# Performance work log

Measured on AMD Instinct MI355X. Metric: run time of the kernel, lower is better.

## Reference

```python
import jax, jax.numpy as jnp
import numpy as np

N = 100000   # nodes
E = 1600000  # edges
IN = 128     # input feature dim
HID = 64     # hidden = IN // 2
OUT = 8      # output_size
B = 16384    # lookup batch


def sage_conv(x, src, dst, W_l, W_r, b, n):
    # PyG SAGEConv (aggr='mean', root_weight=True):
    # out = lin_l(mean_{j in N(i)} x_j) + lin_r(x_i)
    msgs = x[src]                                              # [E, F] gather
    agg = jax.ops.segment_sum(msgs, dst, num_segments=n)       # [N, F] scatter-add
    deg = jax.ops.segment_sum(jnp.ones((src.shape[0],), x.dtype), dst, num_segments=n)
    mean = agg / jnp.maximum(deg, 1.0)[:, None]                # zero-degree -> 0
    return mean @ W_l + x @ W_r + b


def setup_inputs() -> dict:
    key = jax.random.key(0)
    ks = jax.random.split(key, 10)
    node_feats = jax.random.normal(ks[0], (N, IN), dtype=jnp.float32)
    edge_index = jax.random.randint(ks[1], (2, E), 0, N, dtype=jnp.int64)
    idx = jax.random.randint(ks[2], (B,), 0, N, dtype=jnp.int64)
    dropout_mask = jax.random.uniform(ks[3], (N, HID), dtype=jnp.float32)
    s1 = 1.0 / np.sqrt(IN)
    s2 = 1.0 / np.sqrt(HID)
    W1_l = jax.random.normal(ks[4], (IN, HID), dtype=jnp.float32) * s1
    W1_r = jax.random.normal(ks[5], (IN, HID), dtype=jnp.float32) * s1
    b1 = jnp.zeros((HID,), dtype=jnp.float32)
    W2_l = jax.random.normal(ks[6], (HID, OUT), dtype=jnp.float32) * s2
    W2_r = jax.random.normal(ks[7], (HID, OUT), dtype=jnp.float32) * s2
    b2 = jnp.zeros((OUT,), dtype=jnp.float32)
    return {"node_feats": node_feats, "edge_index": edge_index, "idx": idx,
            "dropout_mask": dropout_mask, "W1_l": W1_l, "W1_r": W1_r, "b1": b1,
            "W2_l": W2_l, "W2_r": W2_r, "b2": b2}


def reference(node_feats, edge_index, idx, dropout_mask, W1_l, W1_r, b1, W2_l, W2_r, b2):
    n = node_feats.shape[0]
    src, dst = edge_index[0], edge_index[1]
    h = sage_conv(node_feats, src, dst, W1_l, W1_r, b1, n)     # [N, HID]
    h = jax.nn.relu(h)
    keep = (dropout_mask > 0.5).astype(h.dtype)                # F.dropout p=0.5
    h = h * keep * 2.0                                         # inverted dropout scale 1/(1-p)
    emb = sage_conv(h, src, dst, W2_l, W2_r, b2, n)            # [N, OUT]
    return emb[idx]                                            # [B, OUT]
```

## Files before the change

kernel.cpp:

```cpp
#include <hip/hip_runtime.h>
#include <hip/hip_fp16.h>

#define IN_F 128
#define HID_F 64
#define OUT_F 8

#define BSHIFT 7
#define BGRAN 128
#define BCAP 2688
#define NBUK_MAX 784
#define CHUNK 4096
#define EPT (CHUNK / 256)
#define CEPT ((BCAP + 255) / 256)

typedef _Float16 f16x8 __attribute__((ext_vector_type(8)));
typedef float f32x4 __attribute__((ext_vector_type(4)));

__global__ __launch_bounds__(256) void prep(
    const float* __restrict__ Wl, const float* __restrict__ Wr,
    _Float16* __restrict__ Wt, int* __restrict__ bcur, int nbuk) {
  int blk = blockIdx.x;
  if (blk < 16) {
    int i = blk * 256 + threadIdx.x;
    int n = i & 127;
    int k4 = (i >> 7) * 4;
    _Float16 hv[4];
#pragma unroll
    for (int j = 0; j < 4; ++j) {
      float v = (n < HID_F) ? Wl[(k4 + j) * HID_F + n]
                            : Wr[(k4 + j) * HID_F + (n - HID_F)];
      hv[j] = (_Float16)v;
    }
    *(uint2*)(Wt + (size_t)n * IN_F + k4) = *(uint2*)hv;
  } else {
    for (int i = threadIdx.x; i < nbuk; i += 256) bcur[i] = i * BCAP;
  }
}

__global__ __launch_bounds__(256) void bucket_scatter(
    const int* __restrict__ src, const int* __restrict__ dst,
    int* __restrict__ bcur, int* __restrict__ ebuf, int n_edges) {
  __shared__ int hist[NBUK_MAX];
  __shared__ int base[NBUK_MAX];
  int t = threadIdx.x;
  for (int i = t; i < NBUK_MAX; i += 256) hist[i] = 0;
  __syncthreads();
  int e0 = blockIdx.x * CHUNK;
  int pk[EPT];
  int bk[EPT];
  int rk[EPT];
#pragma unroll
  for (int k = 0; k < EPT; ++k) {
    int e = e0 + k * 256 + t;
    if (e < n_edges) {
      int s = src[e];
      int d = dst[e];
      bk[k] = d >> BSHIFT;
      pk[k] = ((d & (BGRAN - 1)) << 24) | s;
      rk[k] = atomicAdd(&hist[bk[k]], 1);
    } else {
      bk[k] = -1;
    }
  }
  __syncthreads();
  for (int i = t; i < NBUK_MAX; i += 256) {
    int c = hist[i];
    base[i] = c ? atomicAdd(&bcur[i], c) : 0;
  }
  __syncthreads();
#pragma unroll
  for (int k = 0; k < EPT; ++k) {
    if (bk[k] >= 0) ebuf[base[bk[k]] + rk[k]] = pk[k];
  }
}

__global__ __launch_bounds__(256) void bucket_csr(
    const int* __restrict__ ebuf, const int* __restrict__ bcur,
    uint2* __restrict__ nd, int* __restrict__ csr_src, int n_nodes) {
  __shared__ int hist[BGRAN];
  __shared__ int excl_s[BGRAN];
  __shared__ int lds_src[BCAP];
  int b = blockIdx.x;
  int t = threadIdx.x;
  if (t < BGRAN) hist[t] = 0;
  __syncthreads();
  int beg = b * BCAP;
  int cnt = bcur[b] - beg;
  int pk[CEPT];
  int rk[CEPT];
#pragma unroll
  for (int u = 0; u < CEPT; ++u) {
    int j = t + u * 256;
    if (j < cnt) {
      pk[u] = ebuf[beg + j];
      rk[u] = atomicAdd(&hist[(unsigned)pk[u] >> 24], 1);
    } else {
      pk[u] = -1;
    }
  }
  __syncthreads();
  if (t < 64) {
    int h0 = hist[2 * t];
    int h1 = hist[2 * t + 1];
    int ps = h0 + h1;
#pragma unroll
    for (int dd = 1; dd < 64; dd <<= 1) {
      int u = __shfl_up(ps, dd);
      if (t >= dd) ps += u;
    }
    excl_s[2 * t] = ps - h1 - h0;
    excl_s[2 * t + 1] = ps - h1;
  }
  __syncthreads();
  if (t < BGRAN) {
    int node = b * BGRAN + t;
    if (node < n_nodes)
      nd[node] = make_uint2((unsigned)(beg + excl_s[t]), (unsigned)hist[t]);
  }
#pragma unroll
  for (int u = 0; u < CEPT; ++u) {
    if (pk[u] != -1) {
      int bin = (unsigned)pk[u] >> 24;
      lds_src[excl_s[bin] + rk[u]] = pk[u] & 0xFFFFFF;
    }
  }
  __syncthreads();
  for (int j = t; j < cnt; j += 256) csr_src[beg + j] = lds_src[j];
}

#define K1_ROWS 64
#define XSH 136
__global__ __launch_bounds__(256) void k1_proj(
    const float* __restrict__ x,
    const _Float16* __restrict__ Wt,
    const float* __restrict__ b1,
    __half* __restrict__ y1h,
    __half* __restrict__ r1h,
    int n_nodes) {
  __shared__ _Float16 XS[K1_ROWS * XSH];
  int tid = threadIdx.x;
  int w = tid >> 6;
  int lane = tid & 63;
  int n0 = blockIdx.x * K1_ROWS;
  int m = lane & 15;
  int quad = lane >> 4;

  f16x8 af[2][4];
#pragma unroll
  for (int ti = 0; ti < 2; ++ti) {
    int t = w + ti * 4;
#pragma unroll
    for (int kk = 0; kk < 4; ++kk)
      af[ti][kk] = *(const f16x8*)(Wt + (size_t)(t * 16 + m) * IN_F + kk * 32 + quad * 8);
  }
  float4 b1v = *(const float4*)(b1 + w * 16 + quad * 4);

#pragma unroll
  for (int p = 0; p < 8; ++p) {
    int i = tid + p * 256;
    int row = i >> 5;
    int k4 = (i & 31) * 4;
    int gs = min(n0 + row, n_nodes - 1);
    float4 v = *(const float4*)(x + (size_t)gs * IN_F + k4);
    _Float16 hv[4] = {(_Float16)v.x, (_Float16)v.y, (_Float16)v.z, (_Float16)v.w};
    *(uint2*)&XS[row * XSH + k4] = *(uint2*)hv;
  }
  __syncthreads();

#pragma unroll
  for (int rt = 0; rt < 4; ++rt) {
    f32x4 acc0 = f32x4{0.f, 0.f, 0.f, 0.f};
    f32x4 acc1 = f32x4{0.f, 0.f, 0.f, 0.f};
#pragma unroll
    for (int kk = 0; kk < 4; ++kk) {
      f16x8 bx = *(const f16x8*)&XS[(rt * 16 + m) * XSH + kk * 32 + quad * 8];
      acc0 = __builtin_amdgcn_mfma_f32_16x16x32_f16(af[0][kk], bx, acc0, 0, 0, 0);
      acc1 = __builtin_amdgcn_mfma_f32_16x16x32_f16(af[1][kk], bx, acc1, 0, 0, 0);
    }
    int node = n0 + rt * 16 + m;
    if (node < n_nodes) {
      __half hy[4], hr[4];
#pragma unroll
      for (int r = 0; r < 4; ++r) {
        hy[r] = __float2half(acc0[r]);
        hr[r] = __float2half(acc1[r] + ((const float*)&b1v)[r]);
      }
      *(uint2*)(y1h + (size_t)node * HID_F + w * 16 + quad * 4) = *(uint2*)hy;
      *(uint2*)(r1h + (size_t)node * HID_F + w * 16 + quad * 4) = *(uint2*)hr;
    }
  }
}

__global__ __launch_bounds__(256) void agg1_fused(
    const __half* __restrict__ y1h,
    const __half* __restrict__ r1h,
    const uint2* __restrict__ nd,
    const int* __restrict__ csr_src,
    const float* __restrict__ mask,
    __half* __restrict__ h_h,
    int n_nodes) {
  int node = (blockIdx.x * blockDim.x + threadIdx.x) >> 6;
  int lane = threadIdx.x & 63;
  if (node >= n_nodes) return;
  int nu = __builtin_amdgcn_readfirstlane(node);
  int q = lane >> 4;
  int f4 = lane & 15;

  uint2 be = nd[nu];
  size_t o = (size_t)nu * HID_F + f4 * 4;
  uint2 rg = *(const uint2*)(r1h + o);
  float4 mrow = *(const float4*)(mask + (size_t)nu * HID_F + f4 * 4);

  int beg = (int)be.x;
  int d = (int)be.y;
  const int* cp = csr_src + beg;
  const char* yb = (const char*)y1h;
  unsigned foff = (unsigned)(f4 * 8);

  float a0 = 0.f, a1 = 0.f, a2 = 0.f, a3 = 0.f;

#define FLUSH(hx, hy)                       \
  {                                         \
    float2 fx = __half22float2(hx);         \
    float2 fy = __half22float2(hy);         \
    a0 += fx.x; a1 += fx.y;                 \
    a2 += fy.x; a3 += fy.y;                 \
  }

  int j = 0;
  for (; j + 32 <= d; j += 32) {
    unsigned s0 = (unsigned)cp[j + q];
    unsigned s1 = (unsigned)cp[j + 4 + q];
    unsigned s2 = (unsigned)cp[j + 8 + q];
    unsigned s3 = (unsigned)cp[j + 12 + q];
    unsigned s4 = (unsigned)cp[j + 16 + q];
    unsigned s5 = (unsigned)cp[j + 20 + q];
    unsigned s6 = (unsigned)cp[j + 24 + q];
    unsigned s7 = (unsigned)cp[j + 28 + q];
    uint2 g0 = *(const uint2*)(yb + ((s0 << 7) + foff));
    uint2 g1 = *(const uint2*)(yb + ((s1 << 7) + foff));
    uint2 g2 = *(const uint2*)(yb + ((s2 << 7) + foff));
    uint2 g3 = *(const uint2*)(yb + ((s3 << 7) + foff));
    uint2 g4 = *(const uint2*)(yb + ((s4 << 7) + foff));
    uint2 g5 = *(const uint2*)(yb + ((s5 << 7) + foff));
    uint2 g6 = *(const uint2*)(yb + ((s6 << 7) + foff));
    uint2 g7 = *(const uint2*)(yb + ((s7 << 7) + foff));
    __half2 hx = *(const __half2*)&g0.x;
    __half2 hy = *(const __half2*)&g0.y;
    hx = __hadd2(hx, *(const __half2*)&g1.x);
    hy = __hadd2(hy, *(const __half2*)&g1.y);
    hx = __hadd2(hx, *(const __half2*)&g2.x);
    hy = __hadd2(hy, *(const __half2*)&g2.y);
    hx = __hadd2(hx, *(const __half2*)&g3.x);
    hy = __hadd2(hy, *(const __half2*)&g3.y);
    hx = __hadd2(hx, *(const __half2*)&g4.x);
    hy = __hadd2(hy, *(const __half2*)&g4.y);
    hx = __hadd2(hx, *(const __half2*)&g5.x);
    hy = __hadd2(hy, *(const __half2*)&g5.y);
    hx = __hadd2(hx, *(const __half2*)&g6.x);
    hy = __hadd2(hy, *(const __half2*)&g6.y);
    hx = __hadd2(hx, *(const __half2*)&g7.x);
    hy = __hadd2(hy, *(const __half2*)&g7.y);
    FLUSH(hx, hy)
  }
  if (j + 16 <= d) {
    unsigned s0 = (unsigned)cp[j + q];
    unsigned s1 = (unsigned)cp[j + 4 + q];
    unsigned s2 = (unsigned)cp[j + 8 + q];
    unsigned s3 = (unsigned)cp[j + 12 + q];
    uint2 g0 = *(const uint2*)(yb + ((s0 << 7) + foff));
    uint2 g1 = *(const uint2*)(yb + ((s1 << 7) + foff));
    uint2 g2 = *(const uint2*)(yb + ((s2 << 7) + foff));
    uint2 g3 = *(const uint2*)(yb + ((s3 << 7) + foff));
    __half2 hx = *(const __half2*)&g0.x;
    __half2 hy = *(const __half2*)&g0.y;
    hx = __hadd2(hx, *(const __half2*)&g1.x);
    hy = __hadd2(hy, *(const __half2*)&g1.y);
    hx = __hadd2(hx, *(const __half2*)&g2.x);
    hy = __hadd2(hy, *(const __half2*)&g2.y);
    hx = __hadd2(hx, *(const __half2*)&g3.x);
    hy = __hadd2(hy, *(const __half2*)&g3.y);
    FLUSH(hx, hy)
    j += 16;
  }
  if (j < d) {
    int dm = d - 1;
    int e0 = j + q, e1 = j + 4 + q, e2 = j + 8 + q, e3 = j + 12 + q;
    unsigned s0 = (unsigned)cp[min(e0, dm)];
    unsigned s1 = (unsigned)cp[min(e1, dm)];
    unsigned s2 = (unsigned)cp[min(e2, dm)];
    unsigned s3 = (unsigned)cp[min(e3, dm)];
    uint2 g0 = *(const uint2*)(yb + ((s0 << 7) + foff));
    uint2 g1 = *(const uint2*)(yb + ((s1 << 7) + foff));
    uint2 g2 = *(const uint2*)(yb + ((s2 << 7) + foff));
    uint2 g3 = *(const uint2*)(yb + ((s3 << 7) + foff));
    uint2 zz = make_uint2(0u, 0u);
    if (e0 >= d) g0 = zz;
    if (e1 >= d) g1 = zz;
    if (e2 >= d) g2 = zz;
    if (e3 >= d) g3 = zz;
    __half2 hx = *(const __half2*)&g0.x;
    __half2 hy = *(const __half2*)&g0.y;
    hx = __hadd2(hx, *(const __half2*)&g1.x);
    hy = __hadd2(hy, *(const __half2*)&g1.y);
    hx = __hadd2(hx, *(const __half2*)&g2.x);
    hy = __hadd2(hy, *(const __half2*)&g2.y);
    hx = __hadd2(hx, *(const __half2*)&g3.x);
    hy = __hadd2(hy, *(const __half2*)&g3.y);
    FLUSH(hx, hy)
  }
#undef FLUSH

  a0 += __shfl_xor(a0, 16); a0 += __shfl_xor(a0, 32);
  a1 += __shfl_xor(a1, 16); a1 += __shfl_xor(a1, 32);
  a2 += __shfl_xor(a2, 16); a2 += __shfl_xor(a2, 32);
  a3 += __shfl_xor(a3, 16); a3 += __shfl_xor(a3, 32);
  if (q == 0) {
    float inv = 1.0f / fmaxf((float)d, 1.0f);
    float2 r01 = __half22float2(*(const __half2*)&rg.x);
    float2 r23 = __half22float2(*(const __half2*)&rg.y);
    float vx = fmaxf(a0 * inv + r01.x, 0.f);
    float vy = fmaxf(a1 * inv + r01.y, 0.f);
    float vz = fmaxf(a2 * inv + r23.x, 0.f);
    float vw = fmaxf(a3 * inv + r23.y, 0.f);
    vx = (mrow.x > 0.5f) ? vx * 2.f : 0.f;
    vy = (mrow.y > 0.5f) ? vy * 2.f : 0.f;
    vz = (mrow.z > 0.5f) ? vz * 2.f : 0.f;
    vw = (mrow.w > 0.5f) ? vw * 2.f : 0.f;
    __half hh[4] = {__float2half(vx), __float2half(vy),
                    __float2half(vz), __float2half(vw)};
    *(uint2*)(h_h + o) = *(uint2*)hh;
  }
}

__global__ __launch_bounds__(256) void k3b_z(
    const __half* __restrict__ h_h,
    const float* __restrict__ W2l,
    __half* __restrict__ z,
    int n_nodes) {
  __shared__ float WS[HID_F][OUT_F];
  int tid = threadIdx.x;
  if (tid < 128) {
    float4 w = *(const float4*)(W2l + tid * 4);
    *(float4*)&WS[tid >> 1][(tid & 1) * 4] = w;
  }
  __syncthreads();
  int node = blockIdx.x * blockDim.x + tid;
  if (node >= n_nodes) return;
  const __half* hr = h_h + (size_t)node * HID_F;
  float acc[8] = {0, 0, 0, 0, 0, 0, 0, 0};
  for (int k = 0; k < HID_F; k += 8) {
    uint4 hv = *(const uint4*)(hr + k);
    float2 f0 = __half22float2(*(const __half2*)&hv.x);
    float2 f1 = __half22float2(*(const __half2*)&hv.y);
    float2 f2 = __half22float2(*(const __half2*)&hv.z);
    float2 f3 = __half22float2(*(const __half2*)&hv.w);
    float hh[8] = {f0.x, f0.y, f1.x, f1.y, f2.x, f2.y, f3.x, f3.y};
#pragma unroll
    for (int j = 0; j < 8; ++j) {
      float4 w0 = *(const float4*)&WS[k + j][0];
      float4 w1 = *(const float4*)&WS[k + j][4];
      acc[0] += hh[j] * w0.x; acc[1] += hh[j] * w0.y;
      acc[2] += hh[j] * w0.z; acc[3] += hh[j] * w0.w;
      acc[4] += hh[j] * w1.x; acc[5] += hh[j] * w1.y;
      acc[6] += hh[j] * w1.z; acc[7] += hh[j] * w1.w;
    }
  }
  __half hz[8];
#pragma unroll
  for (int j = 0; j < 8; ++j) hz[j] = __float2half(acc[j]);
  *(uint4*)(z + (size_t)node * OUT_F) = *(uint4*)hz;
}

__global__ __launch_bounds__(256) void out_fused(
    const int* __restrict__ idx,
    const __half* __restrict__ z,
    const uint2* __restrict__ nd,
    const int* __restrict__ csr_src,
    const __half* __restrict__ h_h,
    const float* __restrict__ W2r,
    const float* __restrict__ b2,
    float* __restrict__ out,
    int n_batch) {
  int b = (blockIdx.x * blockDim.x + threadIdx.x) >> 6;
  int lane = threadIdx.x & 63;
  if (b >= n_batch) return;
  int bu = __builtin_amdgcn_readfirstlane(b);
  int i = idx[bu];
  int iu = __builtin_amdgcn_readfirstlane(i);
  int e8 = lane >> 3;
  int o = lane & 7;
  uint2 be = nd[iu];
  uint4 hv = *(const uint4*)(h_h + (size_t)iu * HID_F + e8 * 8);
  int beg = (int)be.x;
  int d = (int)be.y;
  const int* cp = csr_src + beg;
  const char* zb = (const char*)z;
  unsigned ooff = (unsigned)(o * 2);
  float acc = 0.f;
  int j = e8;
  for (; j + 8 < d; j += 16) {
    unsigned s0 = (unsigned)cp[j];
    unsigned s1 = (unsigned)cp[j + 8];
    float z0 = __half2float(*(const __half*)(zb + ((s0 << 4) + ooff)));
    float z1 = __half2float(*(const __half*)(zb + ((s1 << 4) + ooff)));
    acc += z0 + z1;
  }
  if (j < d) {
    unsigned s0 = (unsigned)cp[j];
    acc += __half2float(*(const __half*)(zb + ((s0 << 4) + ooff)));
  }
  float dv = fmaxf((float)d, 1.0f);
  float v = acc / dv;
  float2 f0 = __half22float2(*(const __half2*)&hv.x);
  float2 f1 = __half22float2(*(const __half2*)&hv.y);
  float2 f2 = __half22float2(*(const __half2*)&hv.z);
  float2 f3 = __half22float2(*(const __half2*)&hv.w);
  float hh[8] = {f0.x, f0.y, f1.x, f1.y, f2.x, f2.y, f3.x, f3.y};
#pragma unroll
  for (int jj = 0; jj < 8; ++jj) {
    int k = e8 * 8 + jj;
    v += hh[jj] * W2r[k * OUT_F + o];
  }
  v += __shfl_xor(v, 8);
  v += __shfl_xor(v, 16);
  v += __shfl_xor(v, 32);
  if (e8 == 0) out[(size_t)b * OUT_F + o] = v + b2[o];
}

extern "C" void kernel_launch(void* const* d_in, const int* in_sizes, int n_in,
                              void* d_out, int out_size, void* d_ws, size_t ws_size,
                              hipStream_t stream) {
  const float* x    = (const float*)d_in[0];
  const int*   ei   = (const int*)d_in[1];
  const int*   idx  = (const int*)d_in[2];
  const float* mask = (const float*)d_in[3];
  const float* W1l  = (const float*)d_in[4];
  const float* W1r  = (const float*)d_in[5];
  const float* b1   = (const float*)d_in[6];
  const float* W2l  = (const float*)d_in[7];
  const float* W2r  = (const float*)d_in[8];
  const float* b2   = (const float*)d_in[9];
  float* out = (float*)d_out;

  int n_nodes = in_sizes[0] / IN_F;
  int n_edges = in_sizes[1] / 2;
  int n_batch = in_sizes[2];
  const int* src = ei;
  const int* dst = ei + n_edges;

  int nbuk = (n_nodes + BGRAN - 1) / BGRAN;
  int nchunk = (n_edges + CHUNK - 1) / CHUNK;

  char* ws = (char*)d_ws;
  size_t off = 0;
  __half* y1h = (__half*)(ws + off); off += (size_t)n_nodes * HID_F * 2;
  __half* r1h = (__half*)(ws + off); off += (size_t)n_nodes * HID_F * 2;
  __half* h_h = (__half*)(ws + off); off += (size_t)n_nodes * HID_F * 2;
  __half* z   = (__half*)(ws + off); off += (size_t)n_nodes * OUT_F * 2;
  _Float16* Wt = (_Float16*)(ws + off); off += (size_t)IN_F * IN_F * 2;
  int* ebuf    = (int*)(ws + off); off += (size_t)nbuk * BCAP * 4;
  int* csr_src = (int*)(ws + off); off += (size_t)nbuk * BCAP * 4;
  uint2* nd    = (uint2*)(ws + off); off += (size_t)n_nodes * 8;
  int* bcur    = (int*)(ws + off); off += NBUK_MAX * 4;

  prep<<<17, 256, 0, stream>>>(W1l, W1r, Wt, bcur, nbuk);
  bucket_scatter<<<nchunk, 256, 0, stream>>>(src, dst, bcur, ebuf, n_edges);
  k1_proj<<<(n_nodes + K1_ROWS - 1) / K1_ROWS, 256, 0, stream>>>(
      x, Wt, b1, y1h, r1h, n_nodes);
  bucket_csr<<<nbuk, 256, 0, stream>>>(ebuf, bcur, nd, csr_src, n_nodes);

  {
    long long th = (long long)n_nodes * HID_F;
    agg1_fused<<<(int)((th + 255) / 256), 256, 0, stream>>>(
        y1h, r1h, nd, csr_src, mask, h_h, n_nodes);
  }

  k3b_z<<<(n_nodes + 255) / 256, 256, 0, stream>>>(h_h, W2l, z, n_nodes);
  {
    long long th = (long long)n_batch * 64;
    out_fused<<<(int)((th + 255) / 256), 256, 0, stream>>>(
        idx, z, nd, csr_src, h_h, W2r, b2, out, n_batch);
  }
}
```

Measured before the change: 224.0 us.

## Persistent multi-node waves in agg1 with prefetched neighbor indices and packed dropout bits

agg1_fused now runs a fixed pool of waves, each handling several consecutive nodes. It prefetches the next node's CSR range and first 16 neighbor indices while the current node aggregates, to hide index-load latency. The dropout mask is packed into 64-bit bitmasks inside bucket_scatter, so agg1 reads 8 bytes per node instead of 256. The 32-wide unrolled gather loop is reduced to 16-wide, which lowers memory-level parallelism per wave. Fewer waves also means less latency hiding through occupancy.

New measurement: 236.3 us. 1.05x slower.

```diff
diff --git a/kernel.cpp b/kernel.cpp
--- a/kernel.cpp
+++ b/kernel.cpp
@@ -39,7 +39,9 @@
 
 __global__ __launch_bounds__(256) void bucket_scatter(
     const int* __restrict__ src, const int* __restrict__ dst,
-    int* __restrict__ bcur, int* __restrict__ ebuf, int n_edges) {
+    int* __restrict__ bcur, int* __restrict__ ebuf,
+    const float* __restrict__ mask, unsigned long long* __restrict__ mbits,
+    int n_edges, int n_nodes) {
   __shared__ int hist[NBUK_MAX];
   __shared__ int base[NBUK_MAX];
   int t = threadIdx.x;
@@ -71,6 +73,28 @@
 #pragma unroll
   for (int k = 0; k < EPT; ++k) {
     if (bk[k] >= 0) ebuf[base[bk[k]] + rk[k]] = pk[k];
+  }
+
+  int mpb = (n_nodes + (int)gridDim.x - 1) / (int)gridDim.x;
+  int nb0 = blockIdx.x * mpb;
+  int lim = min(nb0 + mpb, n_nodes);
+  int w = t >> 6;
+  int ln = t & 63;
+  for (int nn = nb0 + w * 4; nn < lim; nn += 16) {
+    float m0 = (nn + 0 < lim) ? mask[(size_t)(nn + 0) * HID_F + ln] : 0.f;
+    float m1 = (nn + 1 < lim) ? mask[(size_t)(nn + 1) * HID_F + ln] : 0.f;
+    float m2 = (nn + 2 < lim) ? mask[(size_t)(nn + 2) * HID_F + ln] : 0.f;
+    float m3 = (nn + 3 < lim) ? mask[(size_t)(nn + 3) * HID_F + ln] : 0.f;
+    unsigned long long b0 = __ballot(m0 > 0.5f);
+    unsigned long long b1 = __ballot(m1 > 0.5f);
+    unsigned long long b2 = __ballot(m2 > 0.5f);
+    unsigned long long b3 = __ballot(m3 > 0.5f);
+    if (ln == 0) {
+      if (nn + 0 < lim) mbits[nn + 0] = b0;
+      if (nn + 1 < lim) mbits[nn + 1] = b1;
+      if (nn + 2 < lim) mbits[nn + 2] = b2;
+      if (nn + 3 < lim) mbits[nn + 3] = b3;
+    }
   }
 }
 
@@ -196,141 +220,141 @@
     const __half* __restrict__ r1h,
     const uint2* __restrict__ nd,
     const int* __restrict__ csr_src,
-    const float* __restrict__ mask,
+    const unsigned long long* __restrict__ mbits,
     __half* __restrict__ h_h,
-    int n_nodes) {
-  int node = (blockIdx.x * blockDim.x + threadIdx.x) >> 6;
+    int n_nodes, int npw) {
+  int wid = (blockIdx.x * 256 + threadIdx.x) >> 6;
   int lane = threadIdx.x & 63;
-  if (node >= n_nodes) return;
-  int nu = __builtin_amdgcn_readfirstlane(node);
   int q = lane >> 4;
   int f4 = lane & 15;
-
-  uint2 be = nd[nu];
-  size_t o = (size_t)nu * HID_F + f4 * 4;
-  uint2 rg = *(const uint2*)(r1h + o);
-  float4 mrow = *(const float4*)(mask + (size_t)nu * HID_F + f4 * 4);
-
-  int beg = (int)be.x;
-  int d = (int)be.y;
-  const int* cp = csr_src + beg;
+  int n0 = wid * npw;
+  if (n0 >= n_nodes) return;
+  int nend = min(n0 + npw, n_nodes);
   const char* yb = (const char*)y1h;
   unsigned foff = (unsigned)(f4 * 8);
 
-  float a0 = 0.f, a1 = 0.f, a2 = 0.f, a3 = 0.f;
-
-#define FLUSH(hx, hy)                       \
-  {                                         \
-    float2 fx = __half22float2(hx);         \
-    float2 fy = __half22float2(hy);         \
-    a0 += fx.x; a1 += fx.y;                 \
-    a2 += fy.x; a3 += fy.y;                 \
-  }
-
-  int j = 0;
-  for (; j + 32 <= d; j += 32) {
-    unsigned s0 = (unsigned)cp[j + q];
-    unsigned s1 = (unsigned)cp[j + 4 + q];
-    unsigned s2 = (unsigned)cp[j + 8 + q];
-    unsigned s3 = (unsigned)cp[j + 12 + q];
-    unsigned s4 = (unsigned)cp[j + 16 + q];
-    unsigned s5 = (unsigned)cp[j + 20 + q];
-    unsigned s6 = (unsigned)cp[j + 24 + q];
-    unsigned s7 = (unsigned)cp[j + 28 + q];
-    uint2 g0 = *(const uint2*)(yb + ((s0 << 7) + foff));
-    uint2 g1 = *(const uint2*)(yb + ((s1 << 7) + foff));
-    uint2 g2 = *(const uint2*)(yb + ((s2 << 7) + foff));
-    uint2 g3 = *(const uint2*)(yb + ((s3 << 7) + foff));
-    uint2 g4 = *(const uint2*)(yb + ((s4 << 7) + foff));
-    uint2 g5 = *(const uint2*)(yb + ((s5 << 7) + foff));
-    uint2 g6 = *(const uint2*)(yb + ((s6 << 7) + foff));
-    uint2 g7 = *(const uint2*)(yb + ((s7 << 7) + foff));
-    __half2 hx = *(const __half2*)&g0.x;
-    __half2 hy = *(const __half2*)&g0.y;
-    hx = __hadd2(hx, *(const __half2*)&g1.x);
-    hy = __hadd2(hy, *(const __half2*)&g1.y);
-    hx = __hadd2(hx, *(const __half2*)&g2.x);
-    hy = __hadd2(hy, *(const __half2*)&g2.y);
-    hx = __hadd2(hx, *(const __half2*)&g3.x);
-    hy = __hadd2(hy, *(const __half2*)&g3.y);
-    hx = __hadd2(hx, *(const __half2*)&g4.x);
-    hy = __hadd2(hy, *(const __half2*)&g4.y);
-    hx = __hadd2(hx, *(const __half2*)&g5.x);
-    hy = __hadd2(hy, *(const __half2*)&g5.y);
-    hx = __hadd2(hx, *(const __half2*)&g6.x);
-    hy = __hadd2(hy, *(const __half2*)&g6.y);
-    hx = __hadd2(hx, *(const __half2*)&g7.x);
-    hy = __hadd2(hy, *(const __half2*)&g7.y);
-    FLUSH(hx, hy)
-  }
-  if (j + 16 <= d) {
-    unsigned s0 = (unsigned)cp[j + q];
-    unsigned s1 = (unsigned)cp[j + 4 + q];
-    unsigned s2 = (unsigned)cp[j + 8 + q];
-    unsigned s3 = (unsigned)cp[j + 12 + q];
-    uint2 g0 = *(const uint2*)(yb + ((s0 << 7) + foff));
-    uint2 g1 = *(const uint2*)(yb + ((s1 << 7) + foff));
-    uint2 g2 = *(const uint2*)(yb + ((s2 << 7) + foff));
-    uint2 g3 = *(const uint2*)(yb + ((s3 << 7) + foff));
-    __half2 hx = *(const __half2*)&g0.x;
-    __half2 hy = *(const __half2*)&g0.y;
-    hx = __hadd2(hx, *(const __half2*)&g1.x);
-    hy = __hadd2(hy, *(const __half2*)&g1.y);
-    hx = __hadd2(hx, *(const __half2*)&g2.x);
-    hy = __hadd2(hy, *(const __half2*)&g2.y);
-    hx = __hadd2(hx, *(const __half2*)&g3.x);
-    hy = __hadd2(hy, *(const __half2*)&g3.y);
-    FLUSH(hx, hy)
-    j += 16;
-  }
-  if (j < d) {
-    int dm = d - 1;
-    int e0 = j + q, e1 = j + 4 + q, e2 = j + 8 + q, e3 = j + 12 + q;
-    unsigned s0 = (unsigned)cp[min(e0, dm)];
-    unsigned s1 = (unsigned)cp[min(e1, dm)];
-    unsigned s2 = (unsigned)cp[min(e2, dm)];
-    unsigned s3 = (unsigned)cp[min(e3, dm)];
-    uint2 g0 = *(const uint2*)(yb + ((s0 << 7) + foff));
-    uint2 g1 = *(const uint2*)(yb + ((s1 << 7) + foff));
-    uint2 g2 = *(const uint2*)(yb + ((s2 << 7) + foff));
-    uint2 g3 = *(const uint2*)(yb + ((s3 << 7) + foff));
-    uint2 zz = make_uint2(0u, 0u);
-    if (e0 >= d) g0 = zz;
-    if (e1 >= d) g1 = zz;
-    if (e2 >= d) g2 = zz;
-    if (e3 >= d) g3 = zz;
-    __half2 hx = *(const __half2*)&g0.x;
-    __half2 hy = *(const __half2*)&g0.y;
-    hx = __hadd2(hx, *(const __half2*)&g1.x);
-    hy = __hadd2(hy, *(const __half2*)&g1.y);
-    hx = __hadd2(hx, *(const __half2*)&g2.x);
-    hy = __hadd2(hy, *(const __half2*)&g2.y);
-    hx = __hadd2(hx, *(const __half2*)&g3.x);
-    hy = __hadd2(hy, *(const __half2*)&g3.y);
-    FLUSH(hx, hy)
-  }
-#undef FLUSH
-
-  a0 += __shfl_xor(a0, 16); a0 += __shfl_xor(a0, 32);
-  a1 += __shfl_xor(a1, 16); a1 += __shfl_xor(a1, 32);
-  a2 += __shfl_xor(a2, 16); a2 += __shfl_xor(a2, 32);
-  a3 += __shfl_xor(a3, 16); a3 += __shfl_xor(a3, 32);
-  if (q == 0) {
-    float inv = 1.0f / fmaxf((float)d, 1.0f);
-    float2 r01 = __half22float2(*(const __half2*)&rg.x);
-    float2 r23 = __half22float2(*(const __half2*)&rg.y);
-    float vx = fmaxf(a0 * inv + r01.x, 0.f);
-    float vy = fmaxf(a1 * inv + r01.y, 0.f);
-    float vz = fmaxf(a2 * inv + r23.x, 0.f);
-    float vw = fmaxf(a3 * inv + r23.y, 0.f);
-    vx = (mrow.x > 0.5f) ? vx * 2.f : 0.f;
-    vy = (mrow.y > 0.5f) ? vy * 2.f : 0.f;
-    vz = (mrow.z > 0.5f) ? vz * 2.f : 0.f;
-    vw = (mrow.w > 0.5f) ? vw * 2.f : 0.f;
-    __half hh[4] = {__float2half(vx), __float2half(vy),
-                    __float2half(vz), __float2half(vw)};
-    *(uint2*)(h_h + o) = *(uint2*)hh;
-  }
+#define ACCB(g0, g1, g2, g3)                                 \
+  {                                                          \
+    __half2 hx = *(const __half2*)&(g0).x;                   \
+    __half2 hy = *(const __half2*)&(g0).y;                   \
+    hx = __hadd2(hx, *(const __half2*)&(g1).x);              \
+    hy = __hadd2(hy, *(const __half2*)&(g1).y);              \
+    hx = __hadd2(hx, *(const __half2*)&(g2).x);              \
+    hy = __hadd2(hy, *(const __half2*)&(g2).y);              \
+    hx = __hadd2(hx, *(const __half2*)&(g3).x);              \
+    hy = __hadd2(hy, *(const __half2*)&(g3).y);              \
+    float2 fx = __half22float2(hx);                          \
+    float2 fy = __half22float2(hy);                          \
+    a0 += fx.x; a1 += fx.y; a2 += fy.x; a3 += fy.y;          \
+  }
+
+  int nu0 = __builtin_amdgcn_readfirstlane(n0);
+  uint2 be_c = nd[nu0];
+  unsigned pidx[4] = {0u, 0u, 0u, 0u};
+  {
+    int d0 = (int)be_c.y;
+    if (d0 > 0) {
+      const int* cp0 = csr_src + (int)be_c.x;
+      int dm = d0 - 1;
+#pragma unroll
+      for (int k = 0; k < 4; ++k)
+        pidx[k] = (unsigned)cp0[min(4 * k + q, dm)];
+    }
+  }
+
+  for (int n = n0; n < nend; ++n) {
+    int nu = __builtin_amdgcn_readfirstlane(n);
+    unsigned long long mb = mbits[nu];
+    size_t o = (size_t)nu * HID_F + f4 * 4;
+    uint2 rg = *(const uint2*)(r1h + o);
+    uint2 be_n = make_uint2(0u, 0u);
+    if (n + 1 < nend) {
+      int nun = __builtin_amdgcn_readfirstlane(n + 1);
+      be_n = nd[nun];
+    }
+
+    int d = (int)be_c.y;
+    const int* cp = csr_src + (int)be_c.x;
+    float a0 = 0.f, a1 = 0.f, a2 = 0.f, a3 = 0.f;
+
+    if (d > 0) {
+      uint2 g0 = *(const uint2*)(yb + ((pidx[0] << 7) + foff));
+      uint2 g1 = *(const uint2*)(yb + ((pidx[1] << 7) + foff));
+      uint2 g2 = *(const uint2*)(yb + ((pidx[2] << 7) + foff));
+      uint2 g3 = *(const uint2*)(yb + ((pidx[3] << 7) + foff));
+      uint2 zz = make_uint2(0u, 0u);
+      if (q >= d) g0 = zz;
+      if (4 + q >= d) g1 = zz;
+      if (8 + q >= d) g2 = zz;
+      if (12 + q >= d) g3 = zz;
+      ACCB(g0, g1, g2, g3)
+    }
+    int j = 16;
+    for (; j + 16 <= d; j += 16) {
+      unsigned s0 = (unsigned)cp[j + q];
+      unsigned s1 = (unsigned)cp[j + 4 + q];
+      unsigned s2 = (unsigned)cp[j + 8 + q];
+      unsigned s3 = (unsigned)cp[j + 12 + q];
+      uint2 g0 = *(const uint2*)(yb + ((s0 << 7) + foff));
+      uint2 g1 = *(const uint2*)(yb + ((s1 << 7) + foff));
+      uint2 g2 = *(const uint2*)(yb + ((s2 << 7) + foff));
+      uint2 g3 = *(const uint2*)(yb + ((s3 << 7) + foff));
+      ACCB(g0, g1, g2, g3)
+    }
+    if (j < d) {
+      int dm = d - 1;
+      int e0 = j + q, e1 = j + 4 + q, e2 = j + 8 + q, e3 = j + 12 + q;
+      unsigned s0 = (unsigned)cp[min(e0, dm)];
+      unsigned s1 = (unsigned)cp[min(e1, dm)];
+      unsigned s2 = (unsigned)cp[min(e2, dm)];
+      unsigned s3 = (unsigned)cp[min(e3, dm)];
+      uint2 g0 = *(const uint2*)(yb + ((s0 << 7) + foff));
+      uint2 g1 = *(const uint2*)(yb + ((s1 << 7) + foff));
+      uint2 g2 = *(const uint2*)(yb + ((s2 << 7) + foff));
+      uint2 g3 = *(const uint2*)(yb + ((s3 << 7) + foff));
+      uint2 zz = make_uint2(0u, 0u);
+      if (e0 >= d) g0 = zz;
+      if (e1 >= d) g1 = zz;
+      if (e2 >= d) g2 = zz;
+      if (e3 >= d) g3 = zz;
+      ACCB(g0, g1, g2, g3)
+    }
+
+    if (n + 1 < nend) {
+      int dn = (int)be_n.y;
+      if (dn > 0) {
+        const int* cpn = csr_src + (int)be_n.x;
+        int dmn = dn - 1;
+#pragma unroll
+        for (int k = 0; k < 4; ++k)
+          pidx[k] = (unsigned)cpn[min(4 * k + q, dmn)];
+      }
+    }
+
+    a0 += __shfl_xor(a0, 16); a0 += __shfl_xor(a0, 32);
+    a1 += __shfl_xor(a1, 16); a1 += __shfl_xor(a1, 32);
+    a2 += __shfl_xor(a2, 16); a2 += __shfl_xor(a2, 32);
+    a3 += __shfl_xor(a3, 16); a3 += __shfl_xor(a3, 32);
+    if (q == 0) {
+      float inv = 1.0f / fmaxf((float)d, 1.0f);
+      float2 r01 = __half22float2(*(const __half2*)&rg.x);
+      float2 r23 = __half22float2(*(const __half2*)&rg.y);
+      float vx = fmaxf(a0 * inv + r01.x, 0.f);
+      float vy = fmaxf(a1 * inv + r01.y, 0.f);
+      float vz = fmaxf(a2 * inv + r23.x, 0.f);
+      float vw = fmaxf(a3 * inv + r23.y, 0.f);
+      int fb = f4 * 4;
+      vx = ((mb >> (fb + 0)) & 1ull) ? vx * 2.f : 0.f;
+      vy = ((mb >> (fb + 1)) & 1ull) ? vy * 2.f : 0.f;
+      vz = ((mb >> (fb + 2)) & 1ull) ? vz * 2.f : 0.f;
+      vw = ((mb >> (fb + 3)) & 1ull) ? vw * 2.f : 0.f;
+      __half hh[4] = {__float2half(vx), __float2half(vy),
+                      __float2half(vz), __float2half(vw)};
+      *(uint2*)(h_h + o) = *(uint2*)hh;
+    }
+    be_c = be_n;
+  }
+#undef ACCB
 }
 
 __global__ __launch_bounds__(256) void k3b_z(
@@ -458,6 +482,7 @@
   __half* r1h = (__half*)(ws + off); off += (size_t)n_nodes * HID_F * 2;
   __half* h_h = (__half*)(ws + off); off += (size_t)n_nodes * HID_F * 2;
   __half* z   = (__half*)(ws + off); off += (size_t)n_nodes * OUT_F * 2;
+  unsigned long long* mbits = (unsigned long long*)(ws + off); off += (size_t)n_nodes * 8;
   _Float16* Wt = (_Float16*)(ws + off); off += (size_t)IN_F * IN_F * 2;
   int* ebuf    = (int*)(ws + off); off += (size_t)nbuk * BCAP * 4;
   int* csr_src = (int*)(ws + off); off += (size_t)nbuk * BCAP * 4;
@@ -465,15 +490,19 @@
   int* bcur    = (int*)(ws + off); off += NBUK_MAX * 4;
 
   prep<<<17, 256, 0, stream>>>(W1l, W1r, Wt, bcur, nbuk);
-  bucket_scatter<<<nchunk, 256, 0, stream>>>(src, dst, bcur, ebuf, n_edges);
+  bucket_scatter<<<nchunk, 256, 0, stream>>>(src, dst, bcur, ebuf,
+                                             mask, mbits, n_edges, n_nodes);
   k1_proj<<<(n_nodes + K1_ROWS - 1) / K1_ROWS, 256, 0, stream>>>(
       x, Wt, b1, y1h, r1h, n_nodes);
   bucket_csr<<<nbuk, 256, 0, stream>>>(ebuf, bcur, nd, csr_src, n_nodes);
 
   {
-    long long th = (long long)n_nodes * HID_F;
-    agg1_fused<<<(int)((th + 255) / 256), 256, 0, stream>>>(
-        y1h, r1h, nd, csr_src, mask, h_h, n_nodes);
+    int tw = 8192;
+    int npw = (n_nodes + tw - 1) / tw;
+    int nw = (n_nodes + npw - 1) / npw;
+    int blocks = (nw + 3) / 4;
+    agg1_fused<<<blocks, 256, 0, stream>>>(
+        y1h, r1h, nd, csr_src, mbits, h_h, n_nodes, npw);
   }
 
   k3b_z<<<(n_nodes + 255) / 256, 256, 0, stream>>>(h_h, W2l, z, n_nodes);
```
